# Performance work log

Hardware: AMD Instinct MI355X
Metric: run time of the kernel (lower is better)

## Reference

```python
import jax, jax.numpy as jnp
import numpy as np

N_HEADS = 12


def gconv1x1(x, w, b, groups):
    # x: [B, C, T, S]; w: [O, C//groups] (1x1 kernel squeezed); b: [O]
    B, C, T, S = x.shape
    O, I = w.shape
    xr = x.reshape(B, groups, C // groups, T, S)
    wr = w.reshape(groups, O // groups, I)
    y = jnp.einsum('bgits,goi->bgots', xr, wr).reshape(B, O, T, S)
    return y + b[None, :, None, None]


def setup_inputs() -> dict:
    key = jax.random.key(0)
    ks = jax.random.split(key, 16)
    B, T, E = 2, 512, 768
    H = N_HEADS
    s = 0.02
    inp = {
        'x': jax.random.normal(ks[0], (B, T, E), jnp.float32),
        # fc_q / fc_k / fc_v (torch Linear: y = x @ W.T + b)
        'wq': jax.random.normal(ks[1], (E, E), jnp.float32) * s,
        'bq': jax.random.normal(ks[2], (E,), jnp.float32) * s,
        'wk': jax.random.normal(ks[3], (E, E), jnp.float32) * s,
        'bk': jax.random.normal(ks[4], (E,), jnp.float32) * s,
        'wv': jax.random.normal(ks[5], (E, E), jnp.float32) * s,
        'bv': jax.random.normal(ks[6], (E,), jnp.float32) * s,
        # ConvolutionOp: all 1x1 grouped convs, groups=12
        # conv_inner_subspace_1: in=144 -> out=96  (w: [96, 12])
        'w1': jax.random.normal(ks[7], (8 * H, H), jnp.float32) * s,
        'b1': jax.random.normal(ks[8], (8 * H,), jnp.float32) * s,
        # conv_inner_subspace_2: in=96 -> out=12   (w: [12, 8])
        'w2': jax.random.normal(ks[9], (H, 8), jnp.float32) * s,
        'b2': jax.random.normal(ks[10], (H,), jnp.float32) * s,
        # conv_cross_subspace_1: in=12 -> out=48   (w: [48, 1])
        'w3': jax.random.normal(ks[11], (4 * H, 1), jnp.float32) * s,
        'b3': jax.random.normal(ks[12], (4 * H,), jnp.float32) * s,
        # conv_cross_subspace_2: in=48 -> out=12   (w: [12, 4])
        'w4': jax.random.normal(ks[13], (H, 4), jnp.float32) * s,
        'b4': jax.random.normal(ks[14], (H,), jnp.float32) * s,
    }
    return inp


def reference(x, wq, bq, wk, bk, wv, bv, w1, b1, w2, b2, w3, b3, w4, b4):
    B, T, E = x.shape
    H = N_HEADS
    hd = E // H
    scale = E ** 0.5  # note: sqrt(embed_dim), not sqrt(head_dim)

    def heads(y):  # [B,T,E] -> [H,B,T,hd]
        return y.reshape(B, T, H, hd).transpose(2, 0, 1, 3)

    q = heads(x @ wq.T + bq)
    k = heads(x @ wk.T + bk)
    v = heads(x @ wv.T + bv)

    # all head-pair QK^T: channel index = q_head * H + k_head (matches torch stack order)
    attn = jnp.einsum('qbld,kbtd->qkblt', q, k) / scale          # [H,H,B,T,T]
    attn = attn.transpose(2, 0, 1, 3, 4).reshape(B, H * H, T, T)  # [B,144,T,T]

    # talking-heads style grouped 1x1 conv mixing
    a = jax.nn.relu(gconv1x1(attn, w1, b1, H))   # [B,96,T,T]
    a = gconv1x1(a, w2, b2, H)                    # [B,12,T,T]
    a = jax.nn.relu(gconv1x1(a, w3, b3, H))      # [B,48,T,T]
    a = gconv1x1(a, w4, b4, H)                    # [B,12,T,T]

    # weighted V sum; rearrange 'head b t d -> b t (head d)'
    ctx = jnp.einsum('bhlt,hbtd->blhd', a, v).reshape(B, T, E)
    return ctx
```

## Files before the change

### kernel.cpp

```cpp
#include <hip/hip_runtime.h>

#define DEVINL __device__ __forceinline__

constexpr int E    = 768;
constexpr int TSEQ = 512;
constexpr int NH   = 12;
constexpr int HD   = 64;
constexpr float RSCALE = 0.036084391824351615f;

typedef short bf16x8 __attribute__((ext_vector_type(8)));
typedef float floatx4 __attribute__((ext_vector_type(4)));

DEVINL short f2bf(float x) {
    union { float f; unsigned u; } v; v.f = x;
    unsigned r = v.u + 0x7FFFu + ((v.u >> 16) & 1u);
    return (short)(r >> 16);
}
DEVINL float bf2f(short s) {
    union { unsigned u; float f; } v;
    v.u = ((unsigned)(unsigned short)s) << 16;
    return v.f;
}

DEVINL bf16x8 cvt8(const float* p) {
    float4 f0 = *(const float4*)p;
    float4 f1 = *(const float4*)(p + 4);
    bf16x8 o;
    o[0] = f2bf(f0.x); o[1] = f2bf(f0.y); o[2] = f2bf(f0.z); o[3] = f2bf(f0.w);
    o[4] = f2bf(f1.x); o[5] = f2bf(f1.y); o[6] = f2bf(f1.z); o[7] = f2bf(f1.w);
    return o;
}

__global__ __launch_bounds__(256) void qkv_mfma(
    const float* __restrict__ x,
    const float* __restrict__ wq, const float* __restrict__ bq,
    const float* __restrict__ wk, const float* __restrict__ bk,
    const float* __restrict__ wv, const float* __restrict__ bv,
    short* __restrict__ Qo, short* __restrict__ Ko, short* __restrict__ Vo)
{
    const float* W; const float* bias; short* outp;
    if (blockIdx.z == 0)      { W = wq; bias = bq; outp = Qo; }
    else if (blockIdx.z == 1) { W = wk; bias = bk; outp = Ko; }
    else                      { W = wv; bias = bv; outp = Vo; }

    __shared__ short As[64 * 72];
    __shared__ short Bs[64 * 72];

    const int m0   = blockIdx.x * 64;
    const int n0   = blockIdx.y * 64;
    const int tid  = threadIdx.x;
    const int wvi  = tid >> 6;
    const int lane = tid & 63;
    const int col  = lane & 15;
    const int quad = lane >> 4;

    const int r0 = tid >> 3,   kc0 = tid & 7;
    const int r1 = r0 + 32;

    floatx4 acc[4];
    #pragma unroll
    for (int i = 0; i < 4; i++) acc[i] = (floatx4){0.f, 0.f, 0.f, 0.f};

    bf16x8 a0 = cvt8(&x[(size_t)(m0 + r0) * E + kc0 * 8]);
    bf16x8 a1 = cvt8(&x[(size_t)(m0 + r1) * E + kc0 * 8]);
    bf16x8 b0 = cvt8(&W[(size_t)(n0 + r0) * E + kc0 * 8]);
    bf16x8 b1 = cvt8(&W[(size_t)(n0 + r1) * E + kc0 * 8]);

    for (int k0 = 0; k0 < E; k0 += 64) {
        __syncthreads();
        *(bf16x8*)&As[r0 * 72 + kc0 * 8] = a0;
        *(bf16x8*)&As[r1 * 72 + kc0 * 8] = a1;
        *(bf16x8*)&Bs[r0 * 72 + kc0 * 8] = b0;
        *(bf16x8*)&Bs[r1 * 72 + kc0 * 8] = b1;
        __syncthreads();

        if (k0 + 64 < E) {
            a0 = cvt8(&x[(size_t)(m0 + r0) * E + k0 + 64 + kc0 * 8]);
            a1 = cvt8(&x[(size_t)(m0 + r1) * E + k0 + 64 + kc0 * 8]);
            b0 = cvt8(&W[(size_t)(n0 + r0) * E + k0 + 64 + kc0 * 8]);
            b1 = cvt8(&W[(size_t)(n0 + r1) * E + k0 + 64 + kc0 * 8]);
        }

        #pragma unroll
        for (int k32 = 0; k32 < 2; k32++) {
            bf16x8 bf = *(const bf16x8*)&Bs[(wvi*16 + col) * 72 + k32*32 + quad*8];
            #pragma unroll
            for (int ms = 0; ms < 4; ms++) {
                bf16x8 af = *(const bf16x8*)&As[(ms*16 + col) * 72 + k32*32 + quad*8];
                acc[ms] = __builtin_amdgcn_mfma_f32_16x16x32_bf16(af, bf, acc[ms], 0, 0, 0);
            }
        }
    }

    const float bn = bias[n0 + wvi*16 + col];
    const int h = blockIdx.y;
    #pragma unroll
    for (int ms = 0; ms < 4; ms++) {
        #pragma unroll
        for (int r = 0; r < 4; r++) {
            int m = m0 + ms*16 + quad*4 + r;
            int bb = m >> 9, l = m & 511;
            outp[(((size_t)(bb*NH + h)) * TSEQ + l) * HD + wvi*16 + col] =
                f2bf(acc[ms][r] + bn);
        }
    }
}

__global__ __launch_bounds__(256) void kmix_kernel(
    const short* __restrict__ K,
    const float* __restrict__ w1,
    short* __restrict__ Kp)
{
    const int g  = blockIdx.x * 256 + threadIdx.x;
    const int d8 = g & 7;
    const int t  = (g >> 3) & 511;
    const int o  = (g >> 12) & 7;
    const int bh = g >> 15;
    const int h  = bh % NH;
    const int b  = bh / NH;

    float acc[8] = {};
    #pragma unroll
    for (int i = 0; i < 12; i++) {
        float w = w1[(h*8 + o)*12 + i] * RSCALE;
        bf16x8 kv = *(const bf16x8*)&K[(((size_t)(b*NH + i) * TSEQ) + t) * HD + d8*8];
        #pragma unroll
        for (int j = 0; j < 8; j++)
            acc[j] = fmaf(w, bf2f(kv[j]), acc[j]);
    }
    bf16x8 outv;
    #pragma unroll
    for (int j = 0; j < 8; j++) outv[j] = f2bf(acc[j]);
    *(bf16x8*)&Kp[(size_t)g * 8] = outv;
}

DEVINL float mlp_eval(const float s[8],
                      const float b1r[8], const float w2r[8], float b2r,
                      const float w3r[4], const float b3r[4],
                      const float w4r[4], float b4r)
{
    float z2 = b2r;
    #pragma unroll
    for (int o = 0; o < 8; o++) {
        float z1 = fmaxf(s[o] + b1r[o], 0.0f);
        z2 = fmaf(z1, w2r[o], z2);
    }
    float r = b4r;
    #pragma unroll
    for (int j = 0; j < 4; j++) {
        float z3 = fmaxf(fmaf(z2, w3r[j], b3r[j]), 0.0f);
        r = fmaf(z3, w4r[j], r);
    }
    return r;
}

DEVINL int vrow(int r) { return r*40 + (r >> 3)*8; }

__global__ __launch_bounds__(256, 3) void attn_mfma(
    const short* __restrict__ Qg,
    const short* __restrict__ Kg,
    const short* __restrict__ Vg,
    const float* __restrict__ b1, const float* __restrict__ w2,
    const float* __restrict__ b2, const float* __restrict__ w3,
    const float* __restrict__ b3, const float* __restrict__ w4,
    const float* __restrict__ b4,
    float* __restrict__ Pout)
{
    __shared__ short Ks[256 * 72];
    __shared__ short Vt[2624];
    __shared__ short As[2624];

    const int blk = blockIdx.x;
    const int qtr = blk & 3;
    const int lt  = (blk >> 2) & 7;
    const int bh  = blk >> 5;
    const int h   = bh % NH;
    const int l0  = lt * 64;
    const int tb  = qtr * 128;

    const int tid  = threadIdx.x;
    const int wv   = tid >> 6;
    const int lane = tid & 63;
    const int col  = lane & 15;
    const int quad = lane >> 4;
    const int wl   = wv >> 1;
    const int wt   = wv & 1;

    float b1r[8], w2r[8], w3r[4], b3r[4], w4r[4];
    #pragma unroll
    for (int o = 0; o < 8; o++) { b1r[o] = b1[h*8+o]; w2r[o] = w2[h*8+o]; }
    #pragma unroll
    for (int j = 0; j < 4; j++) { w3r[j] = w3[h*4+j]; b3r[j] = b3[h*4+j]; w4r[j] = w4[h*4+j]; }
    const float b2r = b2[h];
    const float b4r = b4[h];

    bf16x8 qa[2][2];
    {
        const short* qb = Qg + ((size_t)bh * TSEQ + l0 + wl*32 + col) * HD;
        qa[0][0] = *(const bf16x8*)&qb[quad*8];
        qa[0][1] = *(const bf16x8*)&qb[32 + quad*8];
        qa[1][0] = *(const bf16x8*)&qb[16*HD + quad*8];
        qa[1][1] = *(const bf16x8*)&qb[16*HD + 32 + quad*8];
    }

    floatx4 accO[4];
    #pragma unroll
    for (int d16 = 0; d16 < 4; d16++) accO[d16] = (floatx4){0.f, 0.f, 0.f, 0.f};

    const short* kbase = Kg + (size_t)bh * 8 * TSEQ * HD;
    const short* vbase = Vg + (size_t)bh * TSEQ * HD;

    const int tl = tid >> 3;
    const int dc = tid & 7;

    bf16x8 ktmp[8]; bf16x8 vtmp;
    #pragma unroll
    for (int o = 0; o < 8; o++)
        ktmp[o] = *(const bf16x8*)&kbase[((size_t)o * TSEQ + tb + tl) * HD + dc*8];
    vtmp = *(const bf16x8*)&vbase[(size_t)(tb + tl) * HD + dc*8];

    for (int it = 0; it < 4; it++) {
        __syncthreads();

        #pragma unroll
        for (int o = 0; o < 8; o++)
            *(bf16x8*)&Ks[(o*32 + tl)*72 + dc*8] = ktmp[o];
        #pragma unroll
        for (int j = 0; j < 8; j++)
            Vt[vrow(dc*8 + j) + tl] = vtmp[j];

        __syncthreads();

        if (it < 3) {
            const int t1 = tb + (it + 1) * 32;
            #pragma unroll
            for (int o = 0; o < 8; o++)
                ktmp[o] = *(const bf16x8*)&kbase[((size_t)o * TSEQ + t1 + tl) * HD + dc*8];
            vtmp = *(const bf16x8*)&vbase[(size_t)(t1 + tl) * HD + dc*8];
        }

        floatx4 accS[8][2];
        #pragma unroll
        for (int o = 0; o < 8; o++) {
            accS[o][0] = (floatx4){0.f, 0.f, 0.f, 0.f};
            accS[o][1] = (floatx4){0.f, 0.f, 0.f, 0.f};
        }
        #pragma unroll
        for (int k32 = 0; k32 < 2; k32++) {
            #pragma unroll
            for (int o = 0; o < 8; o++) {
                bf16x8 bf = *(const bf16x8*)&Ks[(o*32 + wt*16 + col)*72 + k32*32 + quad*8];
                accS[o][0] = __builtin_amdgcn_mfma_f32_16x16x32_bf16(qa[0][k32], bf, accS[o][0], 0, 0, 0);
                accS[o][1] = __builtin_amdgcn_mfma_f32_16x16x32_bf16(qa[1][k32], bf, accS[o][1], 0, 0, 0);
            }
        }

        #pragma unroll
        for (int li = 0; li < 2; li++) {
            #pragma unroll
            for (int r = 0; r < 4; r++) {
                float s[8];
                #pragma unroll
                for (int o = 0; o < 8; o++) s[o] = accS[o][li][r];
                float a = mlp_eval(s, b1r, w2r, b2r, w3r, b3r, w4r, b4r);
                As[vrow(wl*32 + li*16 + quad*4 + r) + wt*16 + col] = f2bf(a);
            }
        }
        __syncthreads();

        bf16x8 af = *(const bf16x8*)&As[vrow(wv*16 + col) + quad*8];
        #pragma unroll
        for (int d16 = 0; d16 < 4; d16++) {
            bf16x8 vf = *(const bf16x8*)&Vt[vrow(d16*16 + col) + quad*8];
            accO[d16] = __builtin_amdgcn_mfma_f32_16x16x32_bf16(af, vf, accO[d16], 0, 0, 0);
        }
    }

    float* pb = Pout + (size_t)blk * 64 * 64;
    #pragma unroll
    for (int d16 = 0; d16 < 4; d16++)
        #pragma unroll
        for (int r = 0; r < 4; r++)
            pb[(wv*16 + quad*4 + r) * 64 + d16*16 + col] = accO[d16][r];
}

__global__ __launch_bounds__(256) void reduce_kernel(
    const float* __restrict__ P, float* __restrict__ out)
{
    const int gi  = blockIdx.x * 256 + threadIdx.x;
    const int d4  = gi & 15;
    const int r   = (gi >> 4) & 63;
    const int grp = gi >> 10;
    const int lt  = grp & 7;
    const int bh  = grp >> 3;
    const int h   = bh % NH;
    const int b   = bh / NH;

    const float* p0 = P + (size_t)grp * 4 * 4096 + r * 64 + d4 * 4;
    float4 s0 = *(const float4*)&p0[0];
    float4 s1 = *(const float4*)&p0[4096];
    float4 s2 = *(const float4*)&p0[8192];
    float4 s3 = *(const float4*)&p0[12288];
    float4 s;
    s.x = (s0.x + s1.x) + (s2.x + s3.x);
    s.y = (s0.y + s1.y) + (s2.y + s3.y);
    s.z = (s0.z + s1.z) + (s2.z + s3.z);
    s.w = (s0.w + s1.w) + (s2.w + s3.w);
    *(float4*)&out[((size_t)(b*TSEQ + lt*64 + r)) * E + h*64 + d4*4] = s;
}

extern "C" void kernel_launch(void* const* d_in, const int* in_sizes, int n_in,
                              void* d_out, int out_size, void* d_ws, size_t ws_size,
                              hipStream_t stream) {
    const float* x  = (const float*)d_in[0];
    const float* wq = (const float*)d_in[1];
    const float* bq = (const float*)d_in[2];
    const float* wk = (const float*)d_in[3];
    const float* bk = (const float*)d_in[4];
    const float* wv = (const float*)d_in[5];
    const float* bv = (const float*)d_in[6];
    const float* w1 = (const float*)d_in[7];
    const float* b1 = (const float*)d_in[8];
    const float* w2 = (const float*)d_in[9];
    const float* b2 = (const float*)d_in[10];
    const float* w3 = (const float*)d_in[11];
    const float* b3 = (const float*)d_in[12];
    const float* w4 = (const float*)d_in[13];
    const float* b4 = (const float*)d_in[14];
    float* out = (float*)d_out;

    short* Qb = (short*)d_ws;
    short* Kb = Qb + 786432;
    short* Vb = Kb + 786432;
    short* Kp = Vb + 786432;
    float* P  = (float*)(Kp + 6291456);

    qkv_mfma<<<dim3(16, 12, 3), 256, 0, stream>>>(x, wq, bq, wk, bk, wv, bv, Qb, Kb, Vb);
    kmix_kernel<<<3072, 256, 0, stream>>>(Kb, w1, Kp);
    attn_mfma<<<768, 256, 0, stream>>>(Qb, Kp, Vb, b1, w2, b2, w3, b3, w4, b4, P);
    reduce_kernel<<<768, 256, 0, stream>>>(P, out);
}
```

Measured before the change: 145.3 us.

## Remove register prefetch, compute four outputs per thread in kmix, remap attn blocks per XCD

The GEMM and attention kernels drop their software prefetch of the next K/V tile, so loads are issued at the top of each iteration instead of overlapping with MFMA work. In exchange register pressure drops, which may help occupancy. kmix now computes four output channels per thread, reusing each loaded K vector across them, and launches a quarter as many blocks. The attention grid is remapped so each XCD handles contiguous (b,h) groups, aiming for better L2 locality on the chiplet layout.

```diff
diff --git a/kernel.cpp b/kernel.cpp
--- a/kernel.cpp
+++ b/kernel.cpp
@@ -61,26 +61,17 @@
     #pragma unroll
     for (int i = 0; i < 4; i++) acc[i] = (floatx4){0.f, 0.f, 0.f, 0.f};
 
-    bf16x8 a0 = cvt8(&x[(size_t)(m0 + r0) * E + kc0 * 8]);
-    bf16x8 a1 = cvt8(&x[(size_t)(m0 + r1) * E + kc0 * 8]);
-    bf16x8 b0 = cvt8(&W[(size_t)(n0 + r0) * E + kc0 * 8]);
-    bf16x8 b1 = cvt8(&W[(size_t)(n0 + r1) * E + kc0 * 8]);
-
     for (int k0 = 0; k0 < E; k0 += 64) {
+        bf16x8 a0 = cvt8(&x[(size_t)(m0 + r0) * E + k0 + kc0 * 8]);
+        bf16x8 a1 = cvt8(&x[(size_t)(m0 + r1) * E + k0 + kc0 * 8]);
+        bf16x8 b0 = cvt8(&W[(size_t)(n0 + r0) * E + k0 + kc0 * 8]);
+        bf16x8 b1 = cvt8(&W[(size_t)(n0 + r1) * E + k0 + kc0 * 8]);
         __syncthreads();
         *(bf16x8*)&As[r0 * 72 + kc0 * 8] = a0;
         *(bf16x8*)&As[r1 * 72 + kc0 * 8] = a1;
         *(bf16x8*)&Bs[r0 * 72 + kc0 * 8] = b0;
         *(bf16x8*)&Bs[r1 * 72 + kc0 * 8] = b1;
         __syncthreads();
-
-        if (k0 + 64 < E) {
-            a0 = cvt8(&x[(size_t)(m0 + r0) * E + k0 + 64 + kc0 * 8]);
-            a1 = cvt8(&x[(size_t)(m0 + r1) * E + k0 + 64 + kc0 * 8]);
-            b0 = cvt8(&W[(size_t)(n0 + r0) * E + k0 + 64 + kc0 * 8]);
-            b1 = cvt8(&W[(size_t)(n0 + r1) * E + k0 + 64 + kc0 * 8]);
-        }
-
         #pragma unroll
         for (int k32 = 0; k32 < 2; k32++) {
             bf16x8 bf = *(const bf16x8*)&Bs[(wvi*16 + col) * 72 + k32*32 + quad*8];
@@ -114,24 +105,33 @@
     const int g  = blockIdx.x * 256 + threadIdx.x;
     const int d8 = g & 7;
     const int t  = (g >> 3) & 511;
-    const int o  = (g >> 12) & 7;
-    const int bh = g >> 15;
+    const int o2 = (g >> 12) & 1;
+    const int bh = g >> 13;
     const int h  = bh % NH;
     const int b  = bh / NH;
 
-    float acc[8] = {};
+    float acc[4][8] = {};
     #pragma unroll
     for (int i = 0; i < 12; i++) {
-        float w = w1[(h*8 + o)*12 + i] * RSCALE;
         bf16x8 kv = *(const bf16x8*)&K[(((size_t)(b*NH + i) * TSEQ) + t) * HD + d8*8];
-        #pragma unroll
-        for (int j = 0; j < 8; j++)
-            acc[j] = fmaf(w, bf2f(kv[j]), acc[j]);
-    }
-    bf16x8 outv;
-    #pragma unroll
-    for (int j = 0; j < 8; j++) outv[j] = f2bf(acc[j]);
-    *(bf16x8*)&Kp[(size_t)g * 8] = outv;
+        float kf[8];
+        #pragma unroll
+        for (int j = 0; j < 8; j++) kf[j] = bf2f(kv[j]);
+        #pragma unroll
+        for (int oo = 0; oo < 4; oo++) {
+            float w = w1[(h*8 + o2*4 + oo)*12 + i] * RSCALE;
+            #pragma unroll
+            for (int j = 0; j < 8; j++)
+                acc[oo][j] = fmaf(w, kf[j], acc[oo][j]);
+        }
+    }
+    #pragma unroll
+    for (int oo = 0; oo < 4; oo++) {
+        bf16x8 outv;
+        #pragma unroll
+        for (int j = 0; j < 8; j++) outv[j] = f2bf(acc[oo][j]);
+        *(bf16x8*)&Kp[(((size_t)(bh*8 + o2*4 + oo) * TSEQ) + t) * HD + d8*8] = outv;
+    }
 }
 
 DEVINL float mlp_eval(const float s[8],
@@ -170,10 +170,15 @@
     __shared__ short Vt[2624];
     __shared__ short As[2624];
 
-    const int blk = blockIdx.x;
-    const int qtr = blk & 3;
-    const int lt  = (blk >> 2) & 7;
-    const int bh  = blk >> 5;
+    const int hw   = blockIdx.x;
+    const int xcd  = hw & 7;
+    const int slot = hw >> 3;
+    const int bh   = xcd * 3 + (slot >> 5);
+    const int inner= slot & 31;
+    const int lt   = inner >> 2;
+    const int qtr  = inner & 3;
+    const int blk  = (bh * 8 + lt) * 4 + qtr;
+
     const int h   = bh % NH;
     const int l0  = lt * 64;
     const int tb  = qtr * 128;
@@ -213,13 +218,15 @@
     const int tl = tid >> 3;
     const int dc = tid & 7;
 
-    bf16x8 ktmp[8]; bf16x8 vtmp;
-    #pragma unroll
-    for (int o = 0; o < 8; o++)
-        ktmp[o] = *(const bf16x8*)&kbase[((size_t)o * TSEQ + tb + tl) * HD + dc*8];
-    vtmp = *(const bf16x8*)&vbase[(size_t)(tb + tl) * HD + dc*8];
-
     for (int it = 0; it < 4; it++) {
+        const int t0 = tb + it * 32;
+
+        bf16x8 ktmp[8];
+        #pragma unroll
+        for (int o = 0; o < 8; o++)
+            ktmp[o] = *(const bf16x8*)&kbase[((size_t)o * TSEQ + t0 + tl) * HD + dc*8];
+        bf16x8 vtmp = *(const bf16x8*)&vbase[(size_t)(t0 + tl) * HD + dc*8];
+
         __syncthreads();
 
         #pragma unroll
@@ -230,14 +237,6 @@
             Vt[vrow(dc*8 + j) + tl] = vtmp[j];
 
         __syncthreads();
-
-        if (it < 3) {
-            const int t1 = tb + (it + 1) * 32;
-            #pragma unroll
-            for (int o = 0; o < 8; o++)
-                ktmp[o] = *(const bf16x8*)&kbase[((size_t)o * TSEQ + t1 + tl) * HD + dc*8];
-            vtmp = *(const bf16x8*)&vbase[(size_t)(t1 + tl) * HD + dc*8];
-        }
 
         floatx4 accS[8][2];
         #pragma unroll
@@ -336,7 +335,7 @@
     float* P  = (float*)(Kp + 6291456);
 
     qkv_mfma<<<dim3(16, 12, 3), 256, 0, stream>>>(x, wq, bq, wk, bk, wv, bv, Qb, Kb, Vb);
-    kmix_kernel<<<3072, 256, 0, stream>>>(Kb, w1, Kp);
+    kmix_kernel<<<768, 256, 0, stream>>>(Kb, w1, Kp);
     attn_mfma<<<768, 256, 0, stream>>>(Qb, Kp, Vb, b1, w2, b2, w3, b3, w4, b4, P);
     reduce_kernel<<<768, 256, 0, stream>>>(P, out);
 }
```

Result: faster. 138.4 us (-4.7%).
